# Kernel optimization log

Hardware: AMD Instinct MI355X
Metric: run time of the kernel (lower is better)

## Reference

```python
import jax, jax.numpy as jnp
import numpy as np

B, DIM, H, W = 4, 256, 64, 64
DSTATE, EXPAND, DCONV = 64, 2, 4
DINNER = EXPAND * DIM            # 512
HEADDIM = 64
NHEADS = DINNER // HEADDIM       # 8
DINPROJ = 2 * DINNER + 2 * DSTATE + NHEADS   # z, xBC, dt
CONVDIM = DINNER + 2 * DSTATE
EPS = 1e-5


def setup_inputs() -> dict:
    key = jax.random.key(0)
    ks = jax.random.split(key, 12)
    n = lambda i, shape, sc=1.0: jax.random.normal(ks[i], shape, jnp.float32) * sc
    return {
        "x": n(0, (B, DIM, H, W)),
        "Q1": n(1, (B, 1, H, W)),
        "Q2": n(2, (B, 1, H, W)),
        "S": jax.random.uniform(ks[3], (B, 1, H, W), jnp.float32),
        "ln_g": jnp.ones((DIM,), jnp.float32),
        "ln_b": jnp.zeros((DIM,), jnp.float32),
        "W_in": n(4, (DIM, DINPROJ), 0.02),
        "conv_w": n(5, (CONVDIM, DCONV), 0.2),
        "conv_b": jnp.zeros((CONVDIM,), jnp.float32),
        "dt_bias": n(6, (NHEADS,), 0.5),
        "A_log": jnp.log(jnp.linspace(1.0, 8.0, NHEADS)).astype(jnp.float32),
        "Dskip": n(7, (NHEADS,), 0.3) + 1.0,
        "norm_w": jnp.ones((DINNER,), jnp.float32),
        "W_out": n(8, (DINNER, DIM), 0.02),
        "gn_g": jnp.ones((DIM,), jnp.float32),
        "gn_b": jnp.zeros((DIM,), jnp.float32),
        "conv1_w": n(9, (DIM, DIM), 0.05),
    }


def _mamba(seq, W_in, conv_w, conv_b, dt_bias, A_log, Dskip, norm_w, W_out):
    # seq: (Ns, L, D) -- Mamba-2 style SSD forward
    Ns, L, _ = seq.shape
    zxbcdt = seq @ W_in                                   # (Ns,L,DINPROJ)
    z = zxbcdt[..., :DINNER]
    xBC = zxbcdt[..., DINNER:DINNER + CONVDIM]
    dt = zxbcdt[..., DINNER + CONVDIM:]                   # (Ns,L,nh)
    # causal depthwise conv (kernel DCONV) + silu
    xp = jnp.pad(xBC, ((0, 0), (DCONV - 1, 0), (0, 0)))
    xBC = sum(conv_w[:, k] * xp[:, k:k + L, :] for k in range(DCONV)) + conv_b
    xBC = jax.nn.silu(xBC)
    xh = xBC[..., :DINNER].reshape(Ns, L, NHEADS, HEADDIM)
    Bm = xBC[..., DINNER:DINNER + DSTATE]                 # (Ns,L,n) ngroups=1
    Cm = xBC[..., DINNER + DSTATE:]
    dt = jax.nn.softplus(dt + dt_bias)
    A = -jnp.exp(A_log)                                   # (nh,)
    dA = jnp.exp(dt * A)                                  # (Ns,L,nh)
    dBx = jnp.einsum('slh,slhp,sln->slhpn', dt, xh, Bm)   # (Ns,L,nh,hd,n)

    def step(h, inp):
        a, bx, c = inp
        h = a[:, :, None, None] * h + bx                  # (Ns,nh,hd,n)
        return h, jnp.einsum('shpn,sn->shp', h, c)

    h0 = jnp.zeros((Ns, NHEADS, HEADDIM, DSTATE), seq.dtype)
    _, ys = jax.lax.scan(step, h0, (dA.transpose(1, 0, 2),
                                    dBx.transpose(1, 0, 2, 3, 4),
                                    Cm.transpose(1, 0, 2)))
    y = ys.transpose(1, 0, 2, 3) + Dskip[None, None, :, None] * xh
    y = y.reshape(Ns, L, DINNER)
    y = y * jax.nn.silu(z)                                # gated RMSNorm
    y = y * jax.lax.rsqrt(jnp.mean(y * y, axis=-1, keepdims=True) + EPS) * norm_w
    return y @ W_out


def _scan_merge(xn, dim_scan, mp):
    Bb, C, Hh, Ww = xn.shape
    if dim_scan == 3:
        seq = xn.transpose(0, 2, 3, 1).reshape(Bb * Hh, Ww, C)
    else:
        seq = xn.transpose(0, 3, 2, 1).reshape(Bb * Ww, Hh, C)
    fwd = _mamba(seq, *mp)
    bwd = jnp.flip(_mamba(jnp.flip(seq, 1), *mp), 1)
    out = 0.5 * (fwd + bwd)
    if dim_scan == 3:
        return out.reshape(Bb, Hh, Ww, C).transpose(0, 3, 1, 2)
    return out.reshape(Bb, Ww, Hh, C).transpose(0, 3, 2, 1)


def reference(x, Q1, Q2, S, ln_g, ln_b, W_in, conv_w, conv_b, dt_bias, A_log,
              Dskip, norm_w, W_out, gn_g, gn_b, conv1_w):
    # LayerNorm over channel dim
    xt = x.transpose(0, 2, 3, 1)                          # (B,H,W,C)
    mu = xt.mean(-1, keepdims=True)
    var = ((xt - mu) ** 2).mean(-1, keepdims=True)
    xn = ((xt - mu) * jax.lax.rsqrt(var + EPS) * ln_g + ln_b).transpose(0, 3, 1, 2)
    mp = (W_in, conv_w, conv_b, dt_bias, A_log, Dskip, norm_w, W_out)
    f_H = _scan_merge(xn, 3, mp)                          # horizontal (along W)
    f_V = _scan_merge(xn, 2, mp)                          # vertical (along H)
    alpha = jax.nn.sigmoid(Q1)
    fg = (alpha * f_H + (1 - alpha) * f_V) * (0.5 + 0.5 * S)
    # out_proj: Conv1x1 (no bias) + GroupNorm(1) + GELU
    y = jnp.einsum('bchw,oc->bohw', fg, conv1_w)
    mu = y.mean((1, 2, 3), keepdims=True)
    var = ((y - mu) ** 2).mean((1, 2, 3), keepdims=True)
    y = (y - mu) * jax.lax.rsqrt(var + EPS) * gn_g[None, :, None, None] + gn_b[None, :, None, None]
    return jax.nn.gelu(y, approximate=False)
```

## Files before the change

### kernel.cpp

```cpp
#include <hip/hip_runtime.h>
#include <hip/hip_bf16.h>

#define EPSF 1e-5f

typedef unsigned short u16;
typedef __attribute__((ext_vector_type(8))) short short8;
typedef __attribute__((ext_vector_type(4))) float f32x4;

__device__ __forceinline__ float sigf(float x){ return 1.f/(1.f+__expf(-x)); }
__device__ __forceinline__ float siluf(float x){ return x/(1.f+__expf(-x)); }
__device__ __forceinline__ u16 f2bf(float x){ __hip_bfloat16 h = __float2bfloat16(x); return *reinterpret_cast<u16*>(&h); }
__device__ __forceinline__ float bf2f(u16 u){ __hip_bfloat16 h; *reinterpret_cast<u16*>(&h) = u; return __bfloat162float(h); }

union BF8 { short8 v; u16 h[8]; uint4 q; };

__device__ __forceinline__ short8 ldg_frag(const u16* p){
  BF8 u; u.q = *(const uint4*)p; return u.v;
}
#define MFMA16(a,b,c) __builtin_amdgcn_mfma_f32_16x16x32_bf16((a),(b),(c),0,0,0)

__global__ __launch_bounds__(256) void k_ln(const float* __restrict__ x,
                                            const float* __restrict__ g,
                                            const float* __restrict__ b,
                                            u16* __restrict__ xn){
  __shared__ float XL[256][65];
  __shared__ float red[2][4][64];
  __shared__ float muL[64], rsL[64];
  int blk = blockIdx.x; int bb = blk>>6, h = blk&63;
  int t = threadIdx.x;
  const float* xb = x + ((size_t)bb*256*4096) + h*64;
  for(int i=0;i<64;i++){ int idx = t + 256*i; int c = idx>>6, w = idx&63;
    XL[c][w] = xb[(size_t)c*4096 + w]; }
  __syncthreads();
  { int w = t & 63, q = t >> 6;
    float s1=0, s2=0;
    for(int c=q*64;c<q*64+64;c++){ float v = XL[c][w]; s1+=v; s2+=v*v; }
    red[0][q][w]=s1; red[1][q][w]=s2; }
  __syncthreads();
  if(t<64){ float a=0,c2=0;
    for(int q=0;q<4;q++){a+=red[0][q][t]; c2+=red[1][q][t];}
    float mu=a*(1.f/256.f); float var=c2*(1.f/256.f)-mu*mu;
    muL[t]=mu; rsL[t]=rsqrtf(var+EPSF); }
  __syncthreads();
  u16* xnb = xn + (size_t)(bb*64+h)*64*256;
  for(int i=0;i<64;i++){ int idx = t + 256*i; int w = idx>>8, c = idx&255;
    float v = (XL[c][w]-muL[w])*rsL[w]*g[c]+b[c];
    xnb[w*256 + c] = f2bf(v); }
}

__global__ __launch_bounds__(256) void k_prep(const float* __restrict__ Wi,
                                              u16* __restrict__ WiF,
                                              const float* __restrict__ Wo,
                                              const float* __restrict__ W1,
                                              u16* __restrict__ WCF){
  __shared__ float WoL[256];
  int blk = blockIdx.x;
  int t = threadIdx.x;
  if(blk < 146){
    int f = blk*256 + t;
    int lane = f & 63, kk = (f>>6)&7, ji = f>>9;
    int g = lane>>4, c16 = lane&15;
    int j = ji*16 + c16;
    BF8 o;
    #pragma unroll
    for(int i=0;i<8;i++){
      int k = kk*32 + g*8 + i;
      o.h[i] = (j < 1160) ? f2bf(Wi[(size_t)k*1160 + j]) : (u16)0;
    }
    *(uint4*)(WiF + (size_t)f*8) = o.q;
  } else {
    int k = blk - 146;
    int o = t;
    WoL[o] = Wo[(size_t)k*256 + o];
    __syncthreads();
    const float4* w1p = (const float4*)(W1 + (size_t)o*256);
    const float4* wop = (const float4*)WoL;
    float d = 0.f;
    #pragma unroll 8
    for(int i=0;i<64;i++){
      float4 a = wop[i]; float4 b = w1p[i];
      d += a.x*b.x + a.y*b.y + a.z*b.z + a.w*b.w;
    }
    int kk = k>>5, g = (k>>3)&3, i2 = k&7;
    int ci = o>>4, c16 = o&15;
    WCF[(size_t)((((ci*16+kk)*4+g)*16+c16)*8 + i2)] = f2bf(d);
  }
}

__global__ __launch_bounds__(512, 4) void k_gemm_in(const u16* __restrict__ xn,
    const u16* __restrict__ WiF, const float* __restrict__ dtb,
    const float* __restrict__ alog,
    u16* __restrict__ zg, u16* __restrict__ xbc,
    float* __restrict__ dtp, float* __restrict__ dtA){
  __shared__ u16 XL[64][264];
  int cb = blockIdx.x, rb = blockIdx.y;
  int t = threadIdx.x;
  int w = t>>6, lane = t&63, g = lane>>4, c16 = lane&15;

  const u16* asrc = xn + (size_t)rb*64*256;
  #pragma unroll
  for(int i=0;i<4;i++){
    int idx = t + 512*i;
    int row = idx>>5, ch = idx&31;
    *(uint4*)&XL[row][ch*8] = *(const uint4*)(asrc + (size_t)row*256 + ch*8);
  }
  __syncthreads();

  int jbase = cb*15;
  int jcount = (cb==4) ? 13 : 15;
  int jl0 = w*2;

  f32x4 acc[2][4];
  #pragma unroll
  for(int jj=0;jj<2;jj++){
    #pragma unroll
    for(int li=0;li<4;li++) acc[jj][li] = (f32x4){0.f,0.f,0.f,0.f};
  }
  #pragma unroll
  for(int kk=0;kk<8;++kk){
    short8 a0 = *(const short8*)&XL[ 0 + c16][kk*32+g*8];
    short8 a1 = *(const short8*)&XL[16 + c16][kk*32+g*8];
    short8 a2 = *(const short8*)&XL[32 + c16][kk*32+g*8];
    short8 a3 = *(const short8*)&XL[48 + c16][kk*32+g*8];
    #pragma unroll
    for(int jj=0;jj<2;++jj){
      if(jl0+jj < jcount){
        int ji = jbase + jl0 + jj;
        short8 bf = ldg_frag(WiF + ((size_t)(ji*8+kk)*64 + lane)*8);
        acc[jj][0] = MFMA16(a0, bf, acc[jj][0]);
        acc[jj][1] = MFMA16(a1, bf, acc[jj][1]);
        acc[jj][2] = MFMA16(a2, bf, acc[jj][2]);
        acc[jj][3] = MFMA16(a3, bf, acc[jj][3]);
      }
    }
  }
  int mbase = rb*64;
  #pragma unroll
  for(int jj=0;jj<2;++jj){
    if(jl0+jj >= jcount) continue;
    int ji = jbase + jl0 + jj;
    if(ji < 32){
      int col = ji*16 + c16;
      #pragma unroll
      for(int li=0;li<4;li++){
        #pragma unroll
        for(int r2=0;r2<4;r2++)
          zg[(size_t)(mbase + li*16 + g*4 + r2)*512 + col] = f2bf(siluf(acc[jj][li][r2]));
      }
    } else if(ji < 72){
      int col = ji*16 + c16 - 512;
      #pragma unroll
      for(int li=0;li<4;li++){
        #pragma unroll
        for(int r2=0;r2<4;r2++)
          xbc[(size_t)(mbase + li*16 + g*4 + r2)*640 + col] = f2bf(acc[jj][li][r2]);
      }
    } else if(c16 < 8){
      int hd = c16;
      float A = -expf(alog[hd]);
      float bias = dtb[hd];
      #pragma unroll
      for(int li=0;li<4;li++){
        #pragma unroll
        for(int r2=0;r2<4;r2++){
          int m = mbase + li*16 + g*4 + r2;
          float v = acc[jj][li][r2] + bias;
          float sp = (v>20.f)? v : log1pf(expf(v));
          dtp[(size_t)((m>>6)*8 + hd)*64 + (m&63)] = sp;
          dtA[(size_t)((m>>6)*8 + hd)*64 + (m&63)] = sp*A;
        }
      }
    }
  }
}

__global__ __launch_bounds__(640) void k_conv2(const u16* __restrict__ xbc,
    const float* __restrict__ convw, const float* __restrict__ convb,
    u16* __restrict__ xfH, u16* __restrict__ xbH,
    u16* __restrict__ xfV, u16* __restrict__ xbV){
  int s = blockIdx.x, dirV = blockIdx.y;
  int c = threadIdx.x;
  int b = s>>6, r = s&63;
  float4 cw = *(const float4*)(convw + c*4);
  float cb_ = convb[c];
  size_t A0 = dirV ? ((size_t)(b*4096 + r)*640 + c) : ((size_t)s*64*640 + c);
  size_t S  = dirV ? (size_t)64*640 : (size_t)640;
  const u16* pin = xbc + A0;
  u16* pf = (dirV? xfV : xfH) + (size_t)s*64*640 + c;
  u16* pb = (dirV? xbV : xbH) + (size_t)s*64*640 + c;
  float fx1=0.f,fx2=0.f,fx3=0.f, by1=0.f,by2=0.f,by3=0.f;
  #pragma unroll 4
  for(int l=0;l<64;++l){
    float fx0 = bf2f(pin[(size_t)l*S]);
    float by0 = bf2f(pin[(size_t)(63-l)*S]);
    float of = cb_ + cw.w*fx0 + cw.z*fx1 + cw.y*fx2 + cw.x*fx3;
    float ob = cb_ + cw.w*by0 + cw.z*by1 + cw.y*by2 + cw.x*by3;
    pf[l*640] = f2bf(siluf(of));
    pb[l*640] = f2bf(siluf(ob));
    fx3=fx2; fx2=fx1; fx1=fx0;
    by3=by2; by2=by1; by1=by0;
  }
}

__global__ __launch_bounds__(512, 2) void k_scan4(
    const u16* __restrict__ xfH, const u16* __restrict__ xbH,
    const u16* __restrict__ xfV, const u16* __restrict__ xbV,
    const float* __restrict__ dtp_g, const float* __restrict__ dtA_g,
    const float* __restrict__ dskip,
    u16* __restrict__ UH0, u16* __restrict__ UH1,
    u16* __restrict__ UV0, u16* __restrict__ UV1){
  __shared__ __align__(16) char smem[78976];
  u16 (*XV)[520] = (u16(*)[520])smem;
  float* Gtri = (float*)(smem + 66560);
  float* sL   = (float*)(smem + 74880);
  float* dtL  = (float*)(smem + 76928);

  int s = blockIdx.x, y = blockIdx.y, t = threadIdx.x;
  int dirb = y&1, dirV = y>>1;
  int w = t>>6, lane = t&63, g = lane>>4, c16 = lane&15;
  float dsk = dskip[w];
  const u16* xsel = (y==0)? xfH : (y==1)? xbH : (y==2)? xfV : xbV;
  u16* un = ((y==0)? UH0 : (y==1)? UH1 : (y==2)? UV0 : UV1) + (size_t)s*64*512;
  const u16* xb = xsel + (size_t)s*64*640;

  {
    int tt = dirb ? 63-lane : lane;
    size_t dti = dirV ? ((size_t)(((s>>6)*64 + tt)*8 + w))*64 + (s&63)
                      : ((size_t)(s*8 + w))*64 + tt;
    float a = dtA_g[dti];
    float d = dtp_g[dti];
    #pragma unroll
    for(int off=1; off<64; off<<=1){
      float nb = __shfl_up(a, off, 64);
      if(lane >= off) a += nb;
    }
    sL[w*64+lane] = a;
    dtL[w*64+lane] = d;
  }
  #pragma unroll
  for(int tt2=0; tt2<2; ++tt2){
    int tile = 2*w + tt2, li = tile>>2, ji = tile&3;
    f32x4 acc = {0.f,0.f,0.f,0.f};
    #pragma unroll
    for(int kk=0; kk<2; ++kk){
      short8 af = ldg_frag(xb + (size_t)(li*16 + c16)*640 + 576 + kk*32 + g*8);
      short8 bf = ldg_frag(xb + (size_t)(ji*16 + c16)*640 + 512 + kk*32 + g*8);
      acc = MFMA16(af, bf, acc);
    }
    int col = ji*16 + c16;
    #pragma unroll
    for(int r=0;r<4;r++){
      int row = li*16 + g*4 + r;
      if(col <= row) Gtri[(row*(row+1))/2 + col] = acc[r];
    }
  }
  #pragma unroll
  for(int it=0; it<8; ++it){
    int tr = (t>>6) + 8*it;
    int c0 = (t&63)*8;
    uint4 v = *(const uint4*)(xb + (size_t)tr*640 + c0);
    *(uint4*)&XV[tr][c0] = v;
  }
  __syncthreads();
  short8 xfr[4][2];
  #pragma unroll
  for(int pi=0; pi<4; ++pi){
    #pragma unroll
    for(int kk=0; kk<2; ++kk){
      BF8 u;
      #pragma unroll
      for(int i=0;i<8;i++){
        int uu = kk*32 + g*8 + i;
        u.h[i] = XV[uu][w*64 + pi*16 + c16];
      }
      xfr[pi][kk] = u.v;
    }
  }
  #pragma unroll 1
  for(int li=0; li<4; ++li){
    int tr = li*16 + c16;
    float sl = sL[w*64 + tr];
    int tb = (tr*(tr+1))/2;
    short8 mfr[2];
    #pragma unroll
    for(int kk=0; kk<2; ++kk){
      BF8 u;
      #pragma unroll
      for(int i=0;i<8;i++){
        int uu = kk*32 + g*8 + i;
        float m = 0.f;
        if(uu <= tr){
          m = __expf(sl - sL[w*64+uu]) * dtL[w*64+uu] * Gtri[tb + uu];
          if(uu == tr) m += dsk;
        }
        u.h[i] = f2bf(m);
      }
      mfr[kk] = u.v;
    }
    #pragma unroll
    for(int pi=0; pi<4; ++pi){
      f32x4 acc = {0.f,0.f,0.f,0.f};
      acc = MFMA16(mfr[0], xfr[pi][0], acc);
      acc = MFMA16(mfr[1], xfr[pi][1], acc);
      #pragma unroll
      for(int r=0;r<4;r++){
        int trow = li*16 + g*4 + r;
        int lorig = dirb ? 63-trow : trow;
        XV[lorig][w*64 + pi*16 + c16] = f2bf(acc[r]);
      }
    }
  }
  __syncthreads();
  #pragma unroll
  for(int rr=0; rr<8; ++rr){
    int l = w*8 + rr;
    *(uint4*)(un + (size_t)l*512 + lane*8) = *(const uint4*)&XV[l][lane*8];
  }
}

__global__ __launch_bounds__(1024, 4) void k_blendfinal(
    const u16* __restrict__ UH0, const u16* __restrict__ UH1,
    const u16* __restrict__ UV0, const u16* __restrict__ UV1,
    const u16* __restrict__ zg, const float* __restrict__ normw,
    const float* __restrict__ Q1, const float* __restrict__ Sx,
    const u16* __restrict__ WCF,
    float* __restrict__ out, float* __restrict__ stats){
  __shared__ u16 A[64][520];
  __shared__ float asL[64], bsL[64];
  __shared__ float nwL[512];
  __shared__ float red[2][16];
  int blk = blockIdx.x; int bb = blk>>6, h = blk&63;
  int t = threadIdx.x;
  if(t<64){
    float qv = Q1[bb*4096 + h*64 + t];
    float sv = Sx[bb*4096 + h*64 + t];
    float al = sigf(qv);
    float sc = 0.5f + 0.5f*sv;
    asL[t] = al*sc; bsL[t] = (1.f-al)*sc;
  }
  if(t < 512) nwL[t] = normw[t];
  __syncthreads();
  int wv = t>>6, lane = t&63, g = lane>>4, c16 = lane&15;
  #pragma unroll 1
  for(int i=0;i<4;i++){
    int wp = wv + 16*i;
    int c8 = lane*8;
    size_t rH = ((size_t)((bb*64+h)*64 + wp))*512 + c8;
    size_t rV = ((size_t)((bb*64+wp)*64 + h))*512 + c8;
    BF8 h0,h1,v0,v1,z8;
    h0.q = *(const uint4*)(UH0 + rH);
    h1.q = *(const uint4*)(UH1 + rH);
    v0.q = *(const uint4*)(UV0 + rV);
    v1.q = *(const uint4*)(UV1 + rV);
    z8.q = *(const uint4*)(zg  + rH);
    float gh0[8], gh1[8], gv0[8], gv1[8];
    float sh0=0.f, sh1=0.f, sv0=0.f, sv1=0.f;
    #pragma unroll
    for(int j=0;j<8;j++){
      float zv = bf2f(z8.h[j]);
      gh0[j] = bf2f(h0.h[j])*zv; sh0 += gh0[j]*gh0[j];
      gh1[j] = bf2f(h1.h[j])*zv; sh1 += gh1[j]*gh1[j];
      gv0[j] = bf2f(v0.h[j])*zv; sv0 += gv0[j]*gv0[j];
      gv1[j] = bf2f(v1.h[j])*zv; sv1 += gv1[j]*gv1[j];
    }
    #pragma unroll
    for(int off=32; off>=1; off>>=1){
      sh0 += __shfl_xor(sh0, off, 64); sh1 += __shfl_xor(sh1, off, 64);
      sv0 += __shfl_xor(sv0, off, 64); sv1 += __shfl_xor(sv1, off, 64);
    }
    float rh0 = rsqrtf(sh0*(1.f/512.f)+EPSF);
    float rh1 = rsqrtf(sh1*(1.f/512.f)+EPSF);
    float rv0 = rsqrtf(sv0*(1.f/512.f)+EPSF);
    float rv1 = rsqrtf(sv1*(1.f/512.f)+EPSF);
    float aw = 0.5f*asL[wp], bw = 0.5f*bsL[wp];
    BF8 o;
    #pragma unroll
    for(int j=0;j<8;j++){
      float u = nwL[c8+j]*(aw*(gh0[j]*rh0 + gh1[j]*rh1) + bw*(gv0[j]*rv0 + gv1[j]*rv1));
      o.h[j] = f2bf(u);
    }
    *(uint4*)&A[wp][c8] = o.q;
  }
  __syncthreads();
  int ci = wv;
  f32x4 acc0={0.f,0.f,0.f,0.f}, acc1=acc0, acc2=acc0, acc3=acc0;
  #pragma unroll 2
  for(int kk=0; kk<16; ++kk){
    short8 bfr = ldg_frag(WCF + (size_t)((((ci*16+kk)*4+g)*16+c16)*8));
    short8 a0 = *(const short8*)&A[ 0+c16][kk*32+g*8];
    short8 a1 = *(const short8*)&A[16+c16][kk*32+g*8];
    short8 a2 = *(const short8*)&A[32+c16][kk*32+g*8];
    short8 a3 = *(const short8*)&A[48+c16][kk*32+g*8];
    acc0 = MFMA16(a0,bfr,acc0); acc1 = MFMA16(a1,bfr,acc1);
    acc2 = MFMA16(a2,bfr,acc2); acc3 = MFMA16(a3,bfr,acc3);
  }
  float s1=0.f, s2=0.f;
  int o_ = ci*16 + c16;
  #pragma unroll
  for(int li=0; li<4; ++li){
    f32x4 a = (li==0)?acc0 : (li==1)?acc1 : (li==2)?acc2 : acc3;
    int w0 = li*16 + g*4;
    float4 vv = {a[0], a[1], a[2], a[3]};
    s1 += (vv.x+vv.y)+(vv.z+vv.w);
    s2 += (vv.x*vv.x+vv.y*vv.y)+(vv.z*vv.z+vv.w*vv.w);
    *(float4*)(out + (((size_t)(bb*256+o_)*64 + h)*64 + w0)) = vv;
  }
  #pragma unroll
  for(int off=32;off>=1;off>>=1){ s1+=__shfl_xor(s1,off,64); s2+=__shfl_xor(s2,off,64); }
  if(lane==0){ red[0][wv]=s1; red[1][wv]=s2; }
  __syncthreads();
  if(t==0){
    float a=0.f,b=0.f;
    #pragma unroll
    for(int i=0;i<16;i++){ a+=red[0][i]; b+=red[1][i]; }
    stats[blk*2+0]=a; stats[blk*2+1]=b;
  }
}

__global__ __launch_bounds__(256) void k_final(float* __restrict__ out,
    const float* __restrict__ stats, const float* __restrict__ gg,
    const float* __restrict__ gb){
  __shared__ float red[64][2];
  __shared__ float mv[2];
  int blk = blockIdx.x; int bb = blk>>6, h = blk&63;
  int t = threadIdx.x;
  if(t<64){ red[t][0] = stats[(bb*64+t)*2+0]; red[t][1] = stats[(bb*64+t)*2+1]; }
  __syncthreads();
  if(t==0){
    float s1=0.f,s2=0.f;
    for(int i=0;i<64;i++){ s1+=red[i][0]; s2+=red[i][1]; }
    float mu = s1*(1.f/1048576.f);
    float var = s2*(1.f/1048576.f) - mu*mu;
    mv[0]=mu; mv[1]=rsqrtf(var+EPSF);
  }
  __syncthreads();
  float mu = mv[0], rs = mv[1];
  for(int i=0;i<64;i++){ int idx=t+256*i; int o=idx>>6, w=idx&63;
    size_t gidx = (size_t)((bb*256+o)*64+h)*64+w;
    float v = out[gidx];
    float yn = (v-mu)*rs*gg[o] + gb[o];
    out[gidx] = 0.5f*yn*(1.f+erff(yn*0.70710678118654752f));
  }
}

extern "C" void kernel_launch(void* const* d_in, const int* in_sizes, int n_in,
                              void* d_out, int out_size, void* d_ws, size_t ws_size,
                              hipStream_t stream) {
  const float* x     = (const float*)d_in[0];
  const float* Q1    = (const float*)d_in[1];
  const float* Sx    = (const float*)d_in[3];
  const float* lng   = (const float*)d_in[4];
  const float* lnb   = (const float*)d_in[5];
  const float* Wi    = (const float*)d_in[6];
  const float* convw = (const float*)d_in[7];
  const float* convb = (const float*)d_in[8];
  const float* dtb   = (const float*)d_in[9];
  const float* alog  = (const float*)d_in[10];
  const float* dskip = (const float*)d_in[11];
  const float* normw = (const float*)d_in[12];
  const float* Wo    = (const float*)d_in[13];
  const float* gg    = (const float*)d_in[14];
  const float* gb    = (const float*)d_in[15];
  const float* W1    = (const float*)d_in[16];
  float* out = (float*)d_out;
  char* ws = (char*)d_ws;

  size_t o = 0;
  u16*   xnb  = (u16*)(ws + o);  o += (size_t)16384*256*2;
  u16*   zgb  = (u16*)(ws + o);  o += (size_t)16384*512*2;
  u16*   xbc  = (u16*)(ws + o);  o += (size_t)16384*640*2;
  u16*   xfH  = (u16*)(ws + o);  o += (size_t)16384*640*2;
  u16*   xbH  = (u16*)(ws + o);  o += (size_t)16384*640*2;
  u16*   xfV  = (u16*)(ws + o);  o += (size_t)16384*640*2;
  u16*   xbV  = (u16*)(ws + o);  o += (size_t)16384*640*2;
  u16*   UH0  = (u16*)(ws + o);  o += (size_t)16384*512*2;
  u16*   UH1  = (u16*)(ws + o);  o += (size_t)16384*512*2;
  u16*   UV0  = (u16*)(ws + o);  o += (size_t)16384*512*2;
  u16*   UV1  = (u16*)(ws + o);  o += (size_t)16384*512*2;
  float* dtp  = (float*)(ws + o); o += (size_t)131072*4;
  float* dtA  = (float*)(ws + o); o += (size_t)131072*4;
  float* stats= (float*)(ws + o); o += 4096;
  u16*   WiF  = (u16*)(ws + o);  o += (size_t)73*8*64*8*2;
  u16*   WCF  = (u16*)(ws + o);  o += (size_t)16384*8*2;

  k_ln<<<256, 256, 0, stream>>>(x, lng, lnb, xnb);
  k_prep<<<658, 256, 0, stream>>>(Wi, WiF, Wo, W1, WCF);
  k_gemm_in<<<dim3(5,256), 512, 0, stream>>>(xnb, WiF, dtb, alog,
                                             zgb, xbc, dtp, dtA);
  k_conv2<<<dim3(256,2), 640, 0, stream>>>(xbc, convw, convb, xfH, xbH, xfV, xbV);
  k_scan4<<<dim3(256,4), 512, 0, stream>>>(xfH, xbH, xfV, xbV, dtp, dtA, dskip,
                                           UH0, UH1, UV0, UV1);
  k_blendfinal<<<256, 1024, 0, stream>>>(UH0, UH1, UV0, UV1, zgb, normw,
                                         Q1, Sx, WCF, out, stats);
  k_final<<<256, 256, 0, stream>>>(out, stats, gg, gb);
}
```

Measured before the change: 176.1 us.

## Fuse causal depthwise conv and SiLU into scan kernel, drop conv outputs

Removes the separate k_conv2 kernel and its four directional bf16 intermediate buffers. The scan kernel now computes the 4-tap causal conv plus SiLU on the fly from xbc, both for the B/C fragments fed to the MFMA and for the x tile staged into shared memory. This eliminates one launch and a large write-then-read of intermediates. In exchange, each output row re-reads up to four input rows, and the B/C fragment path recomputes the conv redundantly. The vertical direction also reads with strided rows.

```diff
diff --git a/kernel.cpp b/kernel.cpp
--- a/kernel.cpp
+++ b/kernel.cpp
@@ -174,37 +174,35 @@
   }
 }
 
-__global__ __launch_bounds__(640) void k_conv2(const u16* __restrict__ xbc,
+__device__ __forceinline__ short8 conv_frag(const u16* __restrict__ xbc,
+    int s, int dirb, int dirV, int prow, int cbase,
+    const float* __restrict__ convw, const float* __restrict__ convb){
+  int b_ = s>>6, r_ = s&63;
+  BF8 raw[4];
+  #pragma unroll
+  for(int j=0;j<4;j++){
+    int p = prow - 3 + j;
+    if(p >= 0){
+      int po = dirb ? 63-p : p;
+      size_t row = dirV ? ((size_t)b_*4096 + (size_t)po*64 + r_) : ((size_t)s*64 + po);
+      raw[j].q = *(const uint4*)(xbc + row*640 + cbase);
+    } else { raw[j].q.x=0u; raw[j].q.y=0u; raw[j].q.z=0u; raw[j].q.w=0u; }
+  }
+  BF8 o;
+  #pragma unroll
+  for(int i=0;i<8;i++){
+    float4 cw = *(const float4*)(convw + (size_t)(cbase+i)*4);
+    float v = convb[cbase+i]
+            + cw.x*bf2f(raw[0].h[i]) + cw.y*bf2f(raw[1].h[i])
+            + cw.z*bf2f(raw[2].h[i]) + cw.w*bf2f(raw[3].h[i]);
+    o.h[i] = f2bf(siluf(v));
+  }
+  return o.v;
+}
+
+__global__ __launch_bounds__(512, 2) void k_scan4(
+    const u16* __restrict__ xbc,
     const float* __restrict__ convw, const float* __restrict__ convb,
-    u16* __restrict__ xfH, u16* __restrict__ xbH,
-    u16* __restrict__ xfV, u16* __restrict__ xbV){
-  int s = blockIdx.x, dirV = blockIdx.y;
-  int c = threadIdx.x;
-  int b = s>>6, r = s&63;
-  float4 cw = *(const float4*)(convw + c*4);
-  float cb_ = convb[c];
-  size_t A0 = dirV ? ((size_t)(b*4096 + r)*640 + c) : ((size_t)s*64*640 + c);
-  size_t S  = dirV ? (size_t)64*640 : (size_t)640;
-  const u16* pin = xbc + A0;
-  u16* pf = (dirV? xfV : xfH) + (size_t)s*64*640 + c;
-  u16* pb = (dirV? xbV : xbH) + (size_t)s*64*640 + c;
-  float fx1=0.f,fx2=0.f,fx3=0.f, by1=0.f,by2=0.f,by3=0.f;
-  #pragma unroll 4
-  for(int l=0;l<64;++l){
-    float fx0 = bf2f(pin[(size_t)l*S]);
-    float by0 = bf2f(pin[(size_t)(63-l)*S]);
-    float of = cb_ + cw.w*fx0 + cw.z*fx1 + cw.y*fx2 + cw.x*fx3;
-    float ob = cb_ + cw.w*by0 + cw.z*by1 + cw.y*by2 + cw.x*by3;
-    pf[l*640] = f2bf(siluf(of));
-    pb[l*640] = f2bf(siluf(ob));
-    fx3=fx2; fx2=fx1; fx1=fx0;
-    by3=by2; by2=by1; by1=by0;
-  }
-}
-
-__global__ __launch_bounds__(512, 2) void k_scan4(
-    const u16* __restrict__ xfH, const u16* __restrict__ xbH,
-    const u16* __restrict__ xfV, const u16* __restrict__ xbV,
     const float* __restrict__ dtp_g, const float* __restrict__ dtA_g,
     const float* __restrict__ dskip,
     u16* __restrict__ UH0, u16* __restrict__ UH1,
@@ -218,14 +216,13 @@
   int s = blockIdx.x, y = blockIdx.y, t = threadIdx.x;
   int dirb = y&1, dirV = y>>1;
   int w = t>>6, lane = t&63, g = lane>>4, c16 = lane&15;
+  int b_ = s>>6, r_ = s&63;
   float dsk = dskip[w];
-  const u16* xsel = (y==0)? xfH : (y==1)? xbH : (y==2)? xfV : xbV;
   u16* un = ((y==0)? UH0 : (y==1)? UH1 : (y==2)? UV0 : UV1) + (size_t)s*64*512;
-  const u16* xb = xsel + (size_t)s*64*640;
 
   {
     int tt = dirb ? 63-lane : lane;
-    size_t dti = dirV ? ((size_t)(((s>>6)*64 + tt)*8 + w))*64 + (s&63)
+    size_t dti = dirV ? ((size_t)((b_*64 + tt)*8 + w))*64 + r_
                       : ((size_t)(s*8 + w))*64 + tt;
     float a = dtA_g[dti];
     float d = dtp_g[dti];
@@ -243,8 +240,8 @@
     f32x4 acc = {0.f,0.f,0.f,0.f};
     #pragma unroll
     for(int kk=0; kk<2; ++kk){
-      short8 af = ldg_frag(xb + (size_t)(li*16 + c16)*640 + 576 + kk*32 + g*8);
-      short8 bf = ldg_frag(xb + (size_t)(ji*16 + c16)*640 + 512 + kk*32 + g*8);
+      short8 af = conv_frag(xbc, s, dirb, dirV, li*16 + c16, 576 + kk*32 + g*8, convw, convb);
+      short8 bf = conv_frag(xbc, s, dirb, dirV, ji*16 + c16, 512 + kk*32 + g*8, convw, convb);
       acc = MFMA16(af, bf, acc);
     }
     int col = ji*16 + c16;
@@ -254,12 +251,37 @@
       if(col <= row) Gtri[(row*(row+1))/2 + col] = acc[r];
     }
   }
-  #pragma unroll
-  for(int it=0; it<8; ++it){
-    int tr = (t>>6) + 8*it;
-    int c0 = (t&63)*8;
-    uint4 v = *(const uint4*)(xb + (size_t)tr*640 + c0);
-    *(uint4*)&XV[tr][c0] = v;
+  {
+    int c0 = lane*8;
+    float4 cwv[8]; float cbv[8];
+    #pragma unroll
+    for(int i=0;i<8;i++){
+      cwv[i] = *(const float4*)(convw + (size_t)(c0+i)*4);
+      cbv[i] = convb[c0+i];
+    }
+    #pragma unroll
+    for(int it=0; it<8; ++it){
+      int tr = w + 8*it;
+      BF8 raw[4];
+      #pragma unroll
+      for(int j=0;j<4;j++){
+        int p = tr - 3 + j;
+        if(p >= 0){
+          int po = dirb ? 63-p : p;
+          size_t row = dirV ? ((size_t)b_*4096 + (size_t)po*64 + r_) : ((size_t)s*64 + po);
+          raw[j].q = *(const uint4*)(xbc + row*640 + c0);
+        } else { raw[j].q.x=0u; raw[j].q.y=0u; raw[j].q.z=0u; raw[j].q.w=0u; }
+      }
+      BF8 o;
+      #pragma unroll
+      for(int i=0;i<8;i++){
+        float v = cbv[i]
+                + cwv[i].x*bf2f(raw[0].h[i]) + cwv[i].y*bf2f(raw[1].h[i])
+                + cwv[i].z*bf2f(raw[2].h[i]) + cwv[i].w*bf2f(raw[3].h[i]);
+        o.h[i] = f2bf(siluf(v));
+      }
+      *(uint4*)&XV[tr][c0] = o.q;
+    }
   }
   __syncthreads();
   short8 xfr[4][2];
@@ -469,10 +491,6 @@
   u16*   xnb  = (u16*)(ws + o);  o += (size_t)16384*256*2;
   u16*   zgb  = (u16*)(ws + o);  o += (size_t)16384*512*2;
   u16*   xbc  = (u16*)(ws + o);  o += (size_t)16384*640*2;
-  u16*   xfH  = (u16*)(ws + o);  o += (size_t)16384*640*2;
-  u16*   xbH  = (u16*)(ws + o);  o += (size_t)16384*640*2;
-  u16*   xfV  = (u16*)(ws + o);  o += (size_t)16384*640*2;
-  u16*   xbV  = (u16*)(ws + o);  o += (size_t)16384*640*2;
   u16*   UH0  = (u16*)(ws + o);  o += (size_t)16384*512*2;
   u16*   UH1  = (u16*)(ws + o);  o += (size_t)16384*512*2;
   u16*   UV0  = (u16*)(ws + o);  o += (size_t)16384*512*2;
@@ -487,8 +505,7 @@
   k_prep<<<658, 256, 0, stream>>>(Wi, WiF, Wo, W1, WCF);
   k_gemm_in<<<dim3(5,256), 512, 0, stream>>>(xnb, WiF, dtb, alog,
                                              zgb, xbc, dtp, dtA);
-  k_conv2<<<dim3(256,2), 640, 0, stream>>>(xbc, convw, convb, xfH, xbH, xfV, xbV);
-  k_scan4<<<dim3(256,4), 512, 0, stream>>>(xfH, xbH, xfV, xbV, dtp, dtA, dskip,
+  k_scan4<<<dim3(256,4), 512, 0, stream>>>(xbc, convw, convb, dtp, dtA, dskip,
                                            UH0, UH1, UV0, UV1);
   k_blendfinal<<<256, 1024, 0, stream>>>(UH0, UH1, UV0, UV1, zgb, normw,
                                          Q1, Sx, WCF, out, stats);
```

After: 213.9 us. +21.4%, slower.
